# Kernel tuning notes

Measured on AMD Instinct MI355X. Metric: run time of the kernel, lower is better.

The kernel has to match this reference:

```python
import jax, jax.numpy as jnp
import numpy as np

C = 32
C_Z = 128
S = 256
N_SEQ = 256
LN_EPS = 1e-5


def setup_inputs() -> dict:
    key = jax.random.key(0)
    k1, k2, k3, k4 = jax.random.split(key, 4)
    m_si = jax.random.normal(k1, (S, N_SEQ, C), dtype=jnp.float32)
    ln_gamma = jnp.ones((C,), dtype=jnp.float32)
    ln_beta = jnp.zeros((C,), dtype=jnp.float32)
    # nn.Linear(c, 2c, bias=False): weight shape (2c, c)
    W_ab = jax.random.normal(k2, (2 * C, C), dtype=jnp.float32) / np.sqrt(C)
    # nn.Linear(c*c, c_z): weight (c_z, c*c), bias (c_z,)
    W_out = jax.random.normal(k3, (C_Z, C * C), dtype=jnp.float32) / np.sqrt(C * C)
    b_out = jax.random.normal(k4, (C_Z,), dtype=jnp.float32) * 0.01
    return {"m_si": m_si, "ln_gamma": ln_gamma, "ln_beta": ln_beta,
            "W_ab": W_ab, "W_out": W_out, "b_out": b_out}


def reference(m_si, ln_gamma, ln_beta, W_ab, W_out, b_out):
    # LayerNorm over channel dim c
    mu = jnp.mean(m_si, axis=-1, keepdims=True)
    var = jnp.var(m_si, axis=-1, keepdims=True)
    x = (m_si - mu) * jax.lax.rsqrt(var + LN_EPS) * ln_gamma + ln_beta
    # linear_no_bias then chunk into a, b: each (s, n_seq, c)
    ab = jnp.einsum('snc,dc->snd', x, W_ab)
    a, b = ab[..., :C], ab[..., C:]
    # mean over MSA sequences of outer products a[s,i,:] x b[s,j,:]
    # restructured as a contraction over n_seq: (i, j, c, c)
    outer = jnp.einsum('inc,jnd->ijcd', a, b) / N_SEQ
    outer = outer.reshape(S, S, C * C)  # flatten (c, c) -> c*c
    # final linear projection to c_z
    z_ij = jnp.einsum('ijk,zk->ijz', outer, W_out) + b_out
    return z_ij
```

## Files before the change

### kernel.cpp

```cpp
#include <hip/hip_runtime.h>

#define SDIM 256
#define NSEQ 256
#define CDIM 32
#define CZ 128
#define IB 8
#define JB 4

typedef __bf16 bfx8 __attribute__((ext_vector_type(8)));
typedef float fx4 __attribute__((ext_vector_type(4)));
typedef float f32x16 __attribute__((ext_vector_type(16)));
typedef unsigned int u32x4 __attribute__((ext_vector_type(4)));

__device__ __forceinline__ unsigned short f2bf(float f) {
  unsigned int u = __float_as_uint(f);
  u += 0x7fffu + ((u >> 16) & 1u);
  return (unsigned short)(u >> 16);
}

__device__ __forceinline__ unsigned int cvtpk(float lo, float hi) {
  unsigned int r;
  asm("v_cvt_pk_bf16_f32 %0, %1, %2" : "=v"(r) : "v"(lo), "v"(hi));
  return r;
}

__device__ __forceinline__ void gload16(const void* g, void* l) {
  __builtin_amdgcn_global_load_lds((const __attribute__((address_space(1))) unsigned int*)g,
                                   (__attribute__((address_space(3))) unsigned int*)l,
                                   16, 0, 0);
}


__global__ __launch_bounds__(256) void opm_prep(
    const float* __restrict__ m_si, const float* __restrict__ gamma, const float* __restrict__ beta,
    const float* __restrict__ Wab, const float* __restrict__ Wout,
    unsigned short* __restrict__ a_t, unsigned short* __restrict__ b_t,
    unsigned short* __restrict__ w2T)
{
  const int b = blockIdx.x;
  const int t = threadIdx.x;
  if (b < SDIM) {
    __shared__ float wab[2048];
    __shared__ float gbuf[64];
    __shared__ __align__(16) char xbuf[32768];
    float* xin = (float*)xbuf;
    unsigned short* xt = (unsigned short*)xbuf;

    const float* msrc = m_si + b * 8192;
#pragma unroll
    for (int k = 0; k < 8; ++k) ((fx4*)xin)[t + k * 256] = ((const fx4*)msrc)[t + k * 256];
    for (int k = t; k < 2048; k += 256) wab[k] = Wab[k];
    if (t < 32) { gbuf[t] = gamma[t]; gbuf[32 + t] = beta[t]; }
    __syncthreads();

    float x[CDIM];
#pragma unroll
    for (int c = 0; c < CDIM; ++c) x[c] = xin[t * 32 + c];
    __syncthreads();

    float mu = 0.f;
#pragma unroll
    for (int c = 0; c < CDIM; ++c) mu += x[c];
    mu *= (1.f / CDIM);
    float var = 0.f;
#pragma unroll
    for (int c = 0; c < CDIM; ++c) { float d = x[c] - mu; var += d * d; }
    var *= (1.f / CDIM);
    const float inv = rsqrtf(var + 1e-5f);
#pragma unroll
    for (int c = 0; c < CDIM; ++c) x[c] = (x[c] - mu) * inv * gbuf[c] + gbuf[32 + c];

    for (int dp = 0; dp < 64; ++dp) {
      float s = 0.f;
#pragma unroll
      for (int c = 0; c < CDIM; ++c) s += x[c] * wab[dp * 32 + c];
      xt[dp * 256 + t] = f2bf(s);
    }
    __syncthreads();

#pragma unroll
    for (int k = 0; k < 8; ++k) {
      const int q = t + k * 256;
      const int row = q >> 5, cc = q & 31;
      const u32x4 v = *(const u32x4*)(xbuf + row * 512 + cc * 16);
      unsigned short* dst = (row < 32)
        ? (a_t + (b * 32 + row) * 256 + cc * 8)
        : (b_t + (b * 32 + (row - 32)) * 256 + cc * 8);
      *(u32x4*)dst = v;
    }
  } else {
    const int base = ((b - SDIM) * 256 + t) * 64;
#pragma unroll 8
    for (int u = 0; u < 64; ++u) {
      const int dest = base + u;
      const int e  = dest & 7;
      const int zl = (dest >> 3) & 31;
      const int h  = (dest >> 8) & 1;
      const int ks = (dest >> 9) & 63;
      const int zt = dest >> 15;
      const int kp = ks * 16 + h * 8 + e;
      const int c = (kp & 3) | (((kp >> 8) & 1) << 2) | (((kp >> 2) & 1) << 3) | (((kp >> 9) & 1) << 4);
      const int d = (kp >> 3) & 31;
      const int z = zt * 32 + zl;
      w2T[dest] = f2bf(Wout[z * 1024 + c * CDIM + d]);
    }
  }
}

__global__ __launch_bounds__(512, 4) void opm_main(
    const unsigned short* __restrict__ a_t, const unsigned short* __restrict__ b_t,
    const unsigned short* __restrict__ w2T, const float* __restrict__ bout,
    float* __restrict__ out)
{
  __shared__ __align__(16) char smem[65536];
  char* o_sh = smem;

  const int tid = threadIdx.x;
  const int lane = tid & 63;
  const int wid = tid >> 6;
  const int l31 = lane & 31;
  const int h = lane >> 5;

  const int bxr = blockIdx.x;
  const int bx = (bxr & 7) * 256 + (bxr >> 3);
  const int i0 = (bx >> 6) * IB;
  const int j0 = (bx & 63) * JB;

  const int wm = wid >> 1;
  const int wn = wid & 1;
  const int wbase = wid * 1024;

  f32x16 acc00 = {}, acc01 = {}, acc10 = {}, acc11 = {};

  auto STAGE = [&](int buf, int nc) {
    const int nbase = nc * 32;
    char* A = smem + 16384 + buf * 16384;
    char* B = smem + 49152 + buf * 8192;
#pragma unroll
    for (int pass = 0; pass < 2; ++pass) {
      const int q = pass * 512 + tid;
      const int row = q >> 2;
      const int gs = (q & 3) ^ (row & 3);
      const unsigned short* src = a_t + ((i0 + (row >> 5)) * 32 + (row & 31)) * 256 + nbase + gs * 8;
      gload16(src, A + pass * 8192 + wbase);
    }
    {
      const int q = tid;
      const int row = q >> 2;
      const int gs = (q & 3) ^ (row & 3);
      const unsigned short* src = b_t + ((j0 + (row >> 5)) * 32 + (row & 31)) * 256 + nbase + gs * 8;
      gload16(src, B + wbase);
    }
  };

  auto COMPUTE = [&](int buf) {
    char* A = smem + 16384 + buf * 16384;
    char* B = smem + 49152 + buf * 8192;
#pragma unroll
    for (int ks = 0; ks < 2; ++ks) {
      const int s = ks * 2 + h;
      bfx8 af0, af1, bf0, bf1;
      { const int r = wm * 64 + l31;      af0 = *(const bfx8*)(A + r * 64 + ((s ^ (r & 3)) << 4)); }
      { const int r = wm * 64 + 32 + l31; af1 = *(const bfx8*)(A + r * 64 + ((s ^ (r & 3)) << 4)); }
      { const int r = wn * 64 + l31;      bf0 = *(const bfx8*)(B + r * 64 + ((s ^ (r & 3)) << 4)); }
      { const int r = wn * 64 + 32 + l31; bf1 = *(const bfx8*)(B + r * 64 + ((s ^ (r & 3)) << 4)); }
      __builtin_amdgcn_s_setprio(1);
      acc00 = __builtin_amdgcn_mfma_f32_32x32x16_bf16(af0, bf0, acc00, 0, 0, 0);
      acc01 = __builtin_amdgcn_mfma_f32_32x32x16_bf16(af0, bf1, acc01, 0, 0, 0);
      acc10 = __builtin_amdgcn_mfma_f32_32x32x16_bf16(af1, bf0, acc10, 0, 0, 0);
      acc11 = __builtin_amdgcn_mfma_f32_32x32x16_bf16(af1, bf1, acc11, 0, 0, 0);
      __builtin_amdgcn_s_setprio(0);
    }
  };

  STAGE(0, 0);
#pragma unroll 2
  for (int t = 0; t < 8; ++t) {
    if (t < 7) {
      STAGE((t + 1) & 1, t + 1);
      asm volatile("s_waitcnt vmcnt(3)" ::: "memory");
    } else {
      asm volatile("s_waitcnt vmcnt(0)" ::: "memory");
    }
    __builtin_amdgcn_s_barrier();
    asm volatile("" ::: "memory");
    COMPUTE(t & 1);
    asm volatile("s_waitcnt lgkmcnt(0)" ::: "memory");
    __builtin_amdgcn_s_barrier();
  }

  {
    const f32x16 av[4] = { acc00 * 0.00390625f, acc01 * 0.00390625f,
                           acc10 * 0.00390625f, acc11 * 0.00390625f };
#pragma unroll
    for (int mi = 0; mi < 2; ++mi) {
#pragma unroll
      for (int ni = 0; ni < 2; ++ni) {
        const f32x16 a = av[mi * 2 + ni];
        const int p = (wm * 2 + mi) * 4 + (wn * 2 + ni);
#pragma unroll
        for (int c4 = 0; c4 < 2; ++c4) {
          const int sl = l31 + 32 * h + 64 * c4;
          u32x4 v;
          v[0] = cvtpk(a[8 * c4 + 0], a[8 * c4 + 1]);
          v[1] = cvtpk(a[8 * c4 + 2], a[8 * c4 + 3]);
          v[2] = cvtpk(a[8 * c4 + 4], a[8 * c4 + 5]);
          v[3] = cvtpk(a[8 * c4 + 6], a[8 * c4 + 7]);
          *(u32x4*)(o_sh + p * 2048 + ((sl ^ (p & 7)) << 4)) = v;
        }
      }
    }
  }
  __syncthreads();

  {
    const int zt = wid & 3;
    const int kh = wid >> 2;
    const unsigned short* wp = w2T + (zt << 15) + (h << 8) + (l31 << 3);
    f32x16 accB = {};
#pragma unroll 8
    for (int ks2 = 0; ks2 < 32; ++ks2) {
      const int ksg = kh * 32 + ks2;
      const bfx8 wf = *(const bfx8*)(wp + (ksg << 9));
      const int sl = 2 * ksg + h;
      const bfx8 of = *(const bfx8*)(o_sh + l31 * 2048 + ((sl ^ (l31 & 7)) << 4));
      accB = __builtin_amdgcn_mfma_f32_32x32x16_bf16(wf, of, accB, 0, 0, 0);
    }
    __syncthreads();

#pragma unroll
    for (int g2 = 0; g2 < 4; ++g2) {
      fx4 v = { accB[4 * g2], accB[4 * g2 + 1], accB[4 * g2 + 2], accB[4 * g2 + 3] };
      const int s = g2 * 2 + h;
      *(fx4*)(o_sh + kh * 16384 + zt * 4096 + ((s * 32 + l31) << 4)) = v;
    }
  }
  __syncthreads();

#pragma unroll
  for (int k = 0; k < 2; ++k) {
    const int v = tid + k * 512;
    const int zt2 = v >> 8, s2 = (v >> 5) & 7, pp = v & 31;
    const int off = zt2 * 4096 + ((s2 * 32 + pp) << 4);
    fx4 r = *(fx4*)(o_sh + off) + *(fx4*)(o_sh + 16384 + off);
    const int z0 = zt2 * 32 + s2 * 4;
    r += *(const fx4*)(bout + z0);
    const int i = i0 + (pp >> 2), j = j0 + (pp & 3);
    *(fx4*)(out + (i * SDIM + j) * CZ + z0) = r;
  }
}

extern "C" void kernel_launch(void* const* d_in, const int* in_sizes, int n_in,
                              void* d_out, int out_size, void* d_ws, size_t ws_size,
                              hipStream_t stream) {
  const float* m_si  = (const float*)d_in[0];
  const float* gamma = (const float*)d_in[1];
  const float* beta  = (const float*)d_in[2];
  const float* Wab   = (const float*)d_in[3];
  const float* Wout  = (const float*)d_in[4];
  const float* bout  = (const float*)d_in[5];
  float* out = (float*)d_out;

  char* ws = (char*)d_ws;
  unsigned short* a_t = (unsigned short*)ws;
  unsigned short* b_t = (unsigned short*)(ws + (4u << 20));
  unsigned short* w2T = (unsigned short*)(ws + (8u << 20));

  opm_prep<<<dim3(SDIM + 8), dim3(256), 0, stream>>>(m_si, gamma, beta, Wab, Wout, a_t, b_t, w2T);
  opm_main<<<dim3(2048), dim3(512), 0, stream>>>(a_t, b_t, w2T, bout, out);
}
```

Baseline: 90.64 us.

## Split prep blocks by a/b half, pad LDS, change swizzle, prefetch second GEMM

The prep kernel now launches two blocks per sequence row, each computing one half (a or b) of the projection, which doubles parallelism for that stage. The staging buffer is padded to a 36-float stride to avoid LDS bank conflicts. The main kernel's LDS XOR swizzle switches from row&3 to (row>>1)&3 to change the bank-conflict pattern. The second GEMM loop is software-pipelined with one-step register prefetch. In exchange, LayerNorm is computed twice per row, and the full unroll raises register pressure.

```diff
diff --git a/kernel.cpp b/kernel.cpp
--- a/kernel.cpp
+++ b/kernel.cpp
@@ -39,23 +39,28 @@
 {
   const int b = blockIdx.x;
   const int t = threadIdx.x;
-  if (b < SDIM) {
-    __shared__ float wab[2048];
+  if (b < 2 * SDIM) {
+    const int s = b >> 1, dph = b & 1;
+    __shared__ float wab[1024];
     __shared__ float gbuf[64];
-    __shared__ __align__(16) char xbuf[32768];
+    __shared__ __align__(16) char xbuf[36864];
     float* xin = (float*)xbuf;
     unsigned short* xt = (unsigned short*)xbuf;
 
-    const float* msrc = m_si + b * 8192;
-#pragma unroll
-    for (int k = 0; k < 8; ++k) ((fx4*)xin)[t + k * 256] = ((const fx4*)msrc)[t + k * 256];
-    for (int k = t; k < 2048; k += 256) wab[k] = Wab[k];
+    const float* msrc = m_si + s * 8192;
+#pragma unroll
+    for (int k = 0; k < 8; ++k) {
+      const int q = t + k * 256;
+      const int row = q >> 3, cq = q & 7;
+      ((fx4*)xin)[row * 9 + cq] = ((const fx4*)msrc)[q];
+    }
+    for (int k = t; k < 1024; k += 256) wab[k] = Wab[dph * 1024 + k];
     if (t < 32) { gbuf[t] = gamma[t]; gbuf[32 + t] = beta[t]; }
     __syncthreads();
 
     float x[CDIM];
 #pragma unroll
-    for (int c = 0; c < CDIM; ++c) x[c] = xin[t * 32 + c];
+    for (int c = 0; c < CDIM; ++c) x[c] = xin[t * 36 + c];
     __syncthreads();
 
     float mu = 0.f;
@@ -70,26 +75,23 @@
 #pragma unroll
     for (int c = 0; c < CDIM; ++c) x[c] = (x[c] - mu) * inv * gbuf[c] + gbuf[32 + c];
 
-    for (int dp = 0; dp < 64; ++dp) {
-      float s = 0.f;
-#pragma unroll
-      for (int c = 0; c < CDIM; ++c) s += x[c] * wab[dp * 32 + c];
-      xt[dp * 256 + t] = f2bf(s);
-    }
-    __syncthreads();
-
-#pragma unroll
-    for (int k = 0; k < 8; ++k) {
+    for (int dp = 0; dp < 32; ++dp) {
+      float sum = 0.f;
+#pragma unroll
+      for (int c = 0; c < CDIM; ++c) sum += x[c] * wab[dp * 32 + c];
+      xt[dp * 256 + t] = f2bf(sum);
+    }
+    __syncthreads();
+
+    unsigned short* outb = dph ? b_t : a_t;
+#pragma unroll
+    for (int k = 0; k < 4; ++k) {
       const int q = t + k * 256;
       const int row = q >> 5, cc = q & 31;
-      const u32x4 v = *(const u32x4*)(xbuf + row * 512 + cc * 16);
-      unsigned short* dst = (row < 32)
-        ? (a_t + (b * 32 + row) * 256 + cc * 8)
-        : (b_t + (b * 32 + (row - 32)) * 256 + cc * 8);
-      *(u32x4*)dst = v;
+      *(u32x4*)(outb + (s * 32 + row) * 256 + cc * 8) = *(const u32x4*)(xbuf + row * 512 + cc * 16);
     }
   } else {
-    const int base = ((b - SDIM) * 256 + t) * 64;
+    const int base = ((b - 2 * SDIM) * 256 + t) * 64;
 #pragma unroll 8
     for (int u = 0; u < 64; ++u) {
       const int dest = base + u;
@@ -140,14 +142,14 @@
     for (int pass = 0; pass < 2; ++pass) {
       const int q = pass * 512 + tid;
       const int row = q >> 2;
-      const int gs = (q & 3) ^ (row & 3);
+      const int gs = (q & 3) ^ ((q >> 3) & 3);
       const unsigned short* src = a_t + ((i0 + (row >> 5)) * 32 + (row & 31)) * 256 + nbase + gs * 8;
       gload16(src, A + pass * 8192 + wbase);
     }
     {
       const int q = tid;
       const int row = q >> 2;
-      const int gs = (q & 3) ^ (row & 3);
+      const int gs = (q & 3) ^ ((q >> 3) & 3);
       const unsigned short* src = b_t + ((j0 + (row >> 5)) * 32 + (row & 31)) * 256 + nbase + gs * 8;
       gload16(src, B + wbase);
     }
@@ -160,10 +162,10 @@
     for (int ks = 0; ks < 2; ++ks) {
       const int s = ks * 2 + h;
       bfx8 af0, af1, bf0, bf1;
-      { const int r = wm * 64 + l31;      af0 = *(const bfx8*)(A + r * 64 + ((s ^ (r & 3)) << 4)); }
-      { const int r = wm * 64 + 32 + l31; af1 = *(const bfx8*)(A + r * 64 + ((s ^ (r & 3)) << 4)); }
-      { const int r = wn * 64 + l31;      bf0 = *(const bfx8*)(B + r * 64 + ((s ^ (r & 3)) << 4)); }
-      { const int r = wn * 64 + 32 + l31; bf1 = *(const bfx8*)(B + r * 64 + ((s ^ (r & 3)) << 4)); }
+      { const int r = wm * 64 + l31;      af0 = *(const bfx8*)(A + r * 64 + (((s ^ (r >> 1)) & 3) << 4)); }
+      { const int r = wm * 64 + 32 + l31; af1 = *(const bfx8*)(A + r * 64 + (((s ^ (r >> 1)) & 3) << 4)); }
+      { const int r = wn * 64 + l31;      bf0 = *(const bfx8*)(B + r * 64 + (((s ^ (r >> 1)) & 3) << 4)); }
+      { const int r = wn * 64 + 32 + l31; bf1 = *(const bfx8*)(B + r * 64 + (((s ^ (r >> 1)) & 3) << 4)); }
       __builtin_amdgcn_s_setprio(1);
       acc00 = __builtin_amdgcn_mfma_f32_32x32x16_bf16(af0, bf0, acc00, 0, 0, 0);
       acc01 = __builtin_amdgcn_mfma_f32_32x32x16_bf16(af0, bf1, acc01, 0, 0, 0);
@@ -218,14 +220,18 @@
     const int kh = wid >> 2;
     const unsigned short* wp = w2T + (zt << 15) + (h << 8) + (l31 << 3);
     f32x16 accB = {};
-#pragma unroll 8
-    for (int ks2 = 0; ks2 < 32; ++ks2) {
-      const int ksg = kh * 32 + ks2;
-      const bfx8 wf = *(const bfx8*)(wp + (ksg << 9));
-      const int sl = 2 * ksg + h;
-      const bfx8 of = *(const bfx8*)(o_sh + l31 * 2048 + ((sl ^ (l31 & 7)) << 4));
-      accB = __builtin_amdgcn_mfma_f32_32x32x16_bf16(wf, of, accB, 0, 0, 0);
-    }
+    int ksg = kh * 32;
+    bfx8 wfA = *(const bfx8*)(wp + (ksg << 9));
+    bfx8 ofA = *(const bfx8*)(o_sh + l31 * 2048 + (((2 * ksg + h) ^ (l31 & 7)) << 4));
+#pragma unroll
+    for (int it = 0; it < 31; ++it) {
+      const int kn = kh * 32 + it + 1;
+      const bfx8 wfB = *(const bfx8*)(wp + (kn << 9));
+      const bfx8 ofB = *(const bfx8*)(o_sh + l31 * 2048 + (((2 * kn + h) ^ (l31 & 7)) << 4));
+      accB = __builtin_amdgcn_mfma_f32_32x32x16_bf16(wfA, ofA, accB, 0, 0, 0);
+      wfA = wfB; ofA = ofB;
+    }
+    accB = __builtin_amdgcn_mfma_f32_32x32x16_bf16(wfA, ofA, accB, 0, 0, 0);
     __syncthreads();
 
 #pragma unroll
@@ -266,6 +272,6 @@
   unsigned short* b_t = (unsigned short*)(ws + (4u << 20));
   unsigned short* w2T = (unsigned short*)(ws + (8u << 20));
 
-  opm_prep<<<dim3(SDIM + 8), dim3(256), 0, stream>>>(m_si, gamma, beta, Wab, Wout, a_t, b_t, w2T);
+  opm_prep<<<dim3(2 * SDIM + 8), dim3(256), 0, stream>>>(m_si, gamma, beta, Wab, Wout, a_t, b_t, w2T);
   opm_main<<<dim3(2048), dim3(512), 0, stream>>>(a_t, b_t, w2T, bout, out);
 }
```

New measurement: 87.25 us. -3.7%, faster.
